# Performance work log

Hardware: AMD Instinct MI355X
Metric: run time of the kernel (lower is better)

Reference implementation:

```python
import jax, jax.numpy as jnp
import numpy as np

B, S, HID = 2, 2048, 2048
NH, NKV, HD = 16, 4, 128
MAXPOS = 2048


def _rope_tables(features, length, max_timescale=10000.0):
    fraction = jnp.arange(0, features, 2, dtype=jnp.float32) / features
    inv_freq = 1.0 / (max_timescale ** fraction)
    sinusoid = jnp.einsum('i,j->ij', jnp.arange(length, dtype=jnp.float32), inv_freq)
    sinusoid = jnp.concatenate([sinusoid, sinusoid], axis=-1)  # [length, features]
    return jnp.sin(sinusoid), jnp.cos(sinusoid)


def rotate_half(x):
    x1, x2 = jnp.split(x, 2, axis=-1)
    return jnp.concatenate([-x2, x1], axis=-1)


def setup_inputs() -> dict:
    key = jax.random.key(0)
    k1, k2, k3, k4, k5 = jax.random.split(key, 5)
    scale = 1.0 / np.sqrt(HID)
    hidden_states = jax.random.normal(k1, (B, S, HID), dtype=jnp.float32)
    Wq = jax.random.normal(k2, (NH * HD, HID), dtype=jnp.float32) * scale
    Wk = jax.random.normal(k3, (NKV * HD, HID), dtype=jnp.float32) * scale
    Wv = jax.random.normal(k4, (NKV * HD, HID), dtype=jnp.float32) * scale
    Wo = jax.random.normal(k5, (HID, NH * HD), dtype=jnp.float32) * scale
    # causal additive mask [B,1,S,S]
    neg = jnp.finfo(jnp.float32).min
    causal = jnp.where(jnp.tril(jnp.ones((S, S), dtype=bool)), 0.0, neg)
    attention_mask = jnp.broadcast_to(causal[None, None], (B, 1, S, S))
    sin, cos = _rope_tables(HD, MAXPOS)
    return {"hidden_states": hidden_states, "attention_mask": attention_mask,
            "Wq": Wq, "Wk": Wk, "Wv": Wv, "Wo": Wo, "sin": sin, "cos": cos}


def reference(hidden_states, attention_mask, Wq, Wk, Wv, Wo, sin, cos):
    bsz, qlen, _ = hidden_states.shape
    # projections (Linear, no bias): x @ W.T -> [B,S,heads,hd]
    q = (hidden_states @ Wq.T).reshape(bsz, qlen, NH, HD)
    k = (hidden_states @ Wk.T).reshape(bsz, qlen, NKV, HD)
    v = (hidden_states @ Wv.T).reshape(bsz, qlen, NKV, HD)
    # rotary embedding (applied in [B,S,H,D] layout)
    qcos = cos[:qlen][None, :, None, :]
    qsin = sin[:qlen][None, :, None, :]
    q = q * qcos + rotate_half(q) * qsin
    k = k * qcos + rotate_half(k) * qsin
    # GQA: repeat_kv equivalent via einsum grouping; expand kv heads to NH
    n_rep = NH // NKV
    q_g = q.reshape(bsz, qlen, NKV, n_rep, HD)  # group queries per kv head
    # scores: NOTE original applies no 1/sqrt(d) scaling
    scores = jnp.einsum('bqhrd,bkhd->bhrqk', q_g, k).reshape(bsz, NH, qlen, qlen)
    mask = attention_mask.at[:, :, :, 0].set(0.0)
    scores = scores + mask
    probs = jax.nn.softmax(scores.astype(jnp.float32), axis=-1).astype(q.dtype)
    probs_g = probs.reshape(bsz, NKV, n_rep, qlen, qlen)
    out = jnp.einsum('bhrqk,bkhd->bqhrd', probs_g, v).reshape(bsz, qlen, NH * HD)
    return out @ Wo.T
```

## Files before the change

kernel.cpp:

```cpp
#include <hip/hip_runtime.h>
#include <hip/hip_bf16.h>

typedef _Float16 f16x8 __attribute__((ext_vector_type(8)));
typedef __fp16 h16x2 __attribute__((ext_vector_type(2)));
typedef float f32x4 __attribute__((ext_vector_type(4)));
typedef float f32x16 __attribute__((ext_vector_type(16)));

#define B_    2
#define S_    2048
#define HID_  2048
#define NH_   16
#define NKV_  4
#define HD_   128
#define M_TOK 4096
#define NQKV  3072

#define MFMA16(a, b, c) __builtin_amdgcn_mfma_f32_16x16x32_f16(a, b, c, 0, 0, 0)
#define MFMA32(a, b, c) __builtin_amdgcn_mfma_f32_32x32x16_f16(a, b, c, 0, 0, 0)

union UW { unsigned u; h16x2 h; };

__device__ __forceinline__ unsigned short f2h(float f) {
  _Float16 h = (_Float16)f;
  return *(unsigned short*)&h;
}

__device__ __forceinline__ void gload_lds16(const unsigned short* g, unsigned short* l) {
  __builtin_amdgcn_global_load_lds((const __attribute__((address_space(1))) void*)g,
                                   (__attribute__((address_space(3))) void*)l,
                                   16, 0, 0);
}

__global__ void cast_f32_f16(const float* __restrict__ src, unsigned short* __restrict__ dst, int n4) {
  int i = blockIdx.x * blockDim.x + threadIdx.x;
  int stride = gridDim.x * blockDim.x;
  for (int idx = i; idx < n4; idx += stride) {
    float4 v = reinterpret_cast<const float4*>(src)[idx];
    ushort4 o;
    o.x = f2h(v.x); o.y = f2h(v.y); o.z = f2h(v.z); o.w = f2h(v.w);
    reinterpret_cast<ushort4*>(dst)[idx] = o;
  }
}

__global__ void cast_weights(const float* __restrict__ Wq, const float* __restrict__ Wk,
                             const float* __restrict__ Wv, const float* __restrict__ Wo,
                             unsigned short* __restrict__ dst) {
  const int n1 = 2048 * 2048 / 4, n2 = 512 * 2048 / 4;
  const int ntot = n1 * 2 + n2 * 2;
  int i = blockIdx.x * blockDim.x + threadIdx.x;
  int stride = gridDim.x * blockDim.x;
  for (int idx = i; idx < ntot; idx += stride) {
    const float* src; int off;
    if (idx < n1)                { src = Wq; off = idx; }
    else if (idx < n1 + n2)      { src = Wk; off = idx - n1; }
    else if (idx < n1 + 2 * n2)  { src = Wv; off = idx - n1 - n2; }
    else                         { src = Wo; off = idx - n1 - 2 * n2; }
    float4 v = reinterpret_cast<const float4*>(src)[off];
    ushort4 o;
    o.x = f2h(v.x); o.y = f2h(v.y); o.z = f2h(v.z); o.w = f2h(v.w);
    reinterpret_cast<ushort4*>(dst)[idx] = o;
  }
}

#define BM 128
#define BN 128
#define BK 32

template <bool OUT16>
__global__ __launch_bounds__(256) void gemm_bt_f16(
    const unsigned short* __restrict__ A, const unsigned short* __restrict__ Bm,
    void* __restrict__ Cv, int M, int N, int K) {
  __shared__ unsigned short As[BM * BK];
  __shared__ unsigned short Bs[BN * BK];
  const int tid  = threadIdx.x;
  const int lane = tid & 63;
  const int wave = tid >> 6;
  const int nbn  = N / BN;
  const int brow = (blockIdx.x / nbn) * BM;
  const int bcol = (blockIdx.x % nbn) * BN;
  const int wr = (wave >> 1) * 64;
  const int wc = (wave & 1) * 64;

  const int srow = wave * 16 + (lane >> 2);
  const int scol = (lane & 3) * 8;
  const unsigned short* ag = A + (size_t)(brow + srow) * K + scol;
  const unsigned short* bg = Bm + (size_t)(bcol + srow) * K + scol;
  unsigned short* aldsw = As + wave * 512;
  unsigned short* bldsw = Bs + wave * 512;

  f32x4 acc[4][4];
#pragma unroll
  for (int m = 0; m < 4; ++m)
#pragma unroll
    for (int n = 0; n < 4; ++n) acc[m][n] = (f32x4){0.f, 0.f, 0.f, 0.f};

  const int lr = lane & 15;
  const int lg = lane >> 4;

  for (int kt = 0; kt < K; kt += BK) {
    __syncthreads();
    gload_lds16(ag + kt, aldsw);
    gload_lds16(ag + (size_t)64 * K + kt, aldsw + 2048);
    gload_lds16(bg + kt, bldsw);
    gload_lds16(bg + (size_t)64 * K + kt, bldsw + 2048);
    __syncthreads();
    f16x8 af[4], bfr[4];
#pragma unroll
    for (int m = 0; m < 4; ++m)
      af[m] = *reinterpret_cast<const f16x8*>(&As[(wr + m * 16 + lr) * BK + lg * 8]);
#pragma unroll
    for (int n = 0; n < 4; ++n)
      bfr[n] = *reinterpret_cast<const f16x8*>(&Bs[(wc + n * 16 + lr) * BK + lg * 8]);
#pragma unroll
    for (int m = 0; m < 4; ++m)
#pragma unroll
      for (int n = 0; n < 4; ++n)
        acc[m][n] = MFMA16(af[m], bfr[n], acc[m][n]);
  }

#pragma unroll
  for (int m = 0; m < 4; ++m) {
#pragma unroll
    for (int r = 0; r < 4; ++r) {
      int row = brow + wr + m * 16 + lg * 4 + r;
      if (OUT16) {
        unsigned short* cp = (unsigned short*)Cv + (size_t)row * N + bcol + wc + lr;
#pragma unroll
        for (int n = 0; n < 4; ++n) cp[n * 16] = f2h(acc[m][n][r]);
      } else {
        float* cp = (float*)Cv + (size_t)row * N + bcol + wc + lr;
#pragma unroll
        for (int n = 0; n < 4; ++n) cp[n * 16] = acc[m][n][r];
      }
    }
  }
}

__global__ void rope_relayout(const unsigned short* __restrict__ QKV,
                              const float* __restrict__ sin_t, const float* __restrict__ cos_t,
                              unsigned short* __restrict__ Qo, unsigned short* __restrict__ Ko,
                              unsigned short* __restrict__ Vt) {
  int idx = blockIdx.x * blockDim.x + threadIdx.x;
  int d  = idx & 63;
  int t  = idx >> 6;
  int hh = t % 24;
  int bs = t / 24;
  int s  = bs & (S_ - 1);
  int b  = bs >> 11;
  const _Float16* xrow = (const _Float16*)QKV + (size_t)bs * NQKV;
  if (hh < 16) {
    float x0 = (float)xrow[hh * 128 + d], x1 = (float)xrow[hh * 128 + 64 + d];
    float c = cos_t[s * 128 + d], sn = sin_t[s * 128 + d];
    unsigned short* qp = Qo + (((size_t)(b * 16 + hh) * S_) + s) * 128 + d;
    qp[0]  = f2h(x0 * c - x1 * sn);
    qp[64] = f2h(x1 * c + x0 * sn);
  } else if (hh < 20) {
    int kvh = hh - 16;
    float x0 = (float)xrow[2048 + kvh * 128 + d], x1 = (float)xrow[2048 + kvh * 128 + 64 + d];
    float c = cos_t[s * 128 + d], sn = sin_t[s * 128 + d];
    unsigned short* kp = Ko + (((size_t)(b * 4 + kvh) * S_) + s) * 128 + d;
    kp[0]  = f2h(x0 * c - x1 * sn);
    kp[64] = f2h(x1 * c + x0 * sn);
  } else {
    int kvh = hh - 20;
    unsigned short x0 = QKV[(size_t)bs * NQKV + 2560 + kvh * 128 + d];
    unsigned short x1 = QKV[(size_t)bs * NQKV + 2560 + kvh * 128 + 64 + d];
    unsigned short* vp = Vt + ((size_t)(b * 4 + kvh) * 128 + d) * S_ + s;
    vp[0]        = x0;
    vp[64 * S_]  = x1;
  }
}

__global__ __launch_bounds__(256, 2) void flash_attn6(
    const unsigned short* __restrict__ Q, const unsigned short* __restrict__ Kk,
    const unsigned short* __restrict__ Vt, unsigned short* __restrict__ Ao) {
  __shared__ _Float16 Kl[2][64 * 128];
  __shared__ _Float16 Vl[2][128 * 64];
  const int lane = threadIdx.x & 63;
  const int w    = threadIdx.x >> 6;
  const int bh   = blockIdx.x & 31;
  const int bq   = 15 - (int)(blockIdx.x >> 5);
  const int b    = bh >> 4, h = bh & 15, kvh = h >> 2;
  const int q31  = lane & 31;
  const int hi   = lane >> 5;
  const int qb   = bq * 128;
  const int wqb  = qb + w * 32;
  const int qrow = wqb + q31;

  const _Float16* Qp = (const _Float16*)Q + (((size_t)(b * 16 + h) * S_) + qrow) * 128;
  const _Float16* Kp = (const _Float16*)Kk + ((size_t)(b * 4 + kvh) * S_) * 128;
  const _Float16* Vp = (const _Float16*)Vt + ((size_t)(b * 4 + kvh) * 128) * S_;

  f16x8 qf[8];
#pragma unroll
  for (int s = 0; s < 8; ++s) {
    f16x8 t = *reinterpret_cast<const f16x8*>(Qp + s * 16 + hi * 8);
#pragma unroll
    for (int j = 0; j < 8; ++j) t[j] = (_Float16)((float)t[j] * 1.44269504f);
    qf[s] = t;
  }

  f32x16 po0 = {}, po1 = {}, po2 = {}, po3 = {};
  float m = -1e30f, l = 0.f;

  const int krow = (lane >> 4);
  const int vrow = (lane >> 3);
  const int wklim = wqb + 32;
  const int nt = qb / 64 + 2;

#define STAGE(K0S, BUF)                                                               \
  {                                                                                   \
    unsigned short* kdst = (unsigned short*)Kl[BUF] + w * 2048;                       \
    unsigned short* vdst = (unsigned short*)Vl[BUF] + w * 2048;                       \
    _Pragma("unroll") for (int jj = 0; jj < 4; ++jj) {                                \
      const int j = w * 4 + jj;                                                       \
      const int kr = j * 4 + krow;                                                    \
      const int kc = (lane & 15) ^ (kr & 7);                                          \
      gload_lds16((const unsigned short*)(Kp + (size_t)((K0S) + kr) * 128 + kc * 8),  \
                  kdst + jj * 512);                                                   \
      const int vr = j * 8 + vrow;                                                    \
      const int vc = (lane & 7) ^ (vr & 7);                                           \
      gload_lds16((const unsigned short*)(Vp + (size_t)vr * S_ + (K0S) + vc * 8),     \
                  vdst + jj * 512);                                                   \
    }                                                                                 \
  }

  STAGE(0, 0)
  __syncthreads();

  int cur = 0;
  const int r7 = q31 & 7;
  for (int t = 0; t < nt; ++t) {
    const int k0 = t * 64;
    if (t + 1 < nt) STAGE((t + 1) * 64, cur ^ 1)

    if (k0 < wklim) {
      f32x16 s0 = {}, s1 = {};
      const _Float16* Kc = Kl[cur];
      __builtin_amdgcn_s_setprio(1);
#pragma unroll
      for (int s = 0; s < 8; ++s) {
        const int cc = (hi + 2 * s) ^ r7;
        f16x8 kf0 = *reinterpret_cast<const f16x8*>(Kc + q31 * 128 + cc * 8);
        f16x8 kf1 = *reinterpret_cast<const f16x8*>(Kc + (q31 + 32) * 128 + cc * 8);
        s0 = MFMA32(kf0, qf[s], s0);
        s1 = MFMA32(kf1, qf[s], s1);
      }
      __builtin_amdgcn_s_setprio(0);

      if (k0 + 63 > wqb) {
        int qrel = qrow - k0 - 4 * hi;
#pragma unroll
        for (int r = 0; r < 16; ++r) {
          int cr = (r & 3) + 8 * (r >> 2);
          if (cr > qrel)      s0[r] = -1e30f;
          if (cr + 32 > qrel) s1[r] = -1e30f;
        }
      }
      float tmx[8];
#pragma unroll
      for (int r = 0; r < 8; ++r)
        tmx[r] = fmaxf(fmaxf(s0[r], s0[r + 8]), fmaxf(s1[r], s1[r + 8]));
#pragma unroll
      for (int d = 4; d > 0; d >>= 1)
#pragma unroll
        for (int r = 0; r < d; ++r) tmx[r] = fmaxf(tmx[r], tmx[r + d]);
      float pmax = fmaxf(tmx[0], __shfl_xor(tmx[0], 32));
      if (__any(pmax > m + 8.0f)) {
        float mn = fmaxf(m, pmax);
        float sc = __builtin_amdgcn_exp2f(m - mn);
        l *= sc;
#pragma unroll
        for (int r = 0; r < 16; ++r) {
          po0[r] *= sc; po1[r] *= sc; po2[r] *= sc; po3[r] *= sc;
        }
        m = mn;
      }
#pragma unroll
      for (int r = 0; r < 16; ++r) s0[r] = __builtin_amdgcn_exp2f(s0[r] - m);
#pragma unroll
      for (int r = 0; r < 16; ++r) s1[r] = __builtin_amdgcn_exp2f(s1[r] - m);
      float u[8];
#pragma unroll
      for (int r = 0; r < 8; ++r)
        u[r] = (s0[r] + s0[r + 8]) + (s1[r] + s1[r + 8]);
#pragma unroll
      for (int d = 4; d > 0; d >>= 1)
#pragma unroll
        for (int r = 0; r < d; ++r) u[r] += u[r + d];
      l += u[0] + __shfl_xor(u[0], 32);

      f16x8 pa[4];
#pragma unroll
      for (int sl = 0; sl < 4; ++sl) {
        f32x16 sv = (sl < 2) ? s0 : s1;
        const int R = (sl & 1) * 8;
        UW w00, w01, w10, w11;
        w00.h = __builtin_amdgcn_cvt_pkrtz(sv[R + 0], sv[R + 1]);
        w01.h = __builtin_amdgcn_cvt_pkrtz(sv[R + 2], sv[R + 3]);
        w10.h = __builtin_amdgcn_cvt_pkrtz(sv[R + 4], sv[R + 5]);
        w11.h = __builtin_amdgcn_cvt_pkrtz(sv[R + 6], sv[R + 7]);
        unsigned x00 = __shfl_xor(w00.u, 32);
        unsigned x01 = __shfl_xor(w01.u, 32);
        unsigned x10 = __shfl_xor(w10.u, 32);
        unsigned x11 = __shfl_xor(w11.u, 32);
        UW W0, W1, W2, W3;
        W0.u = hi ? x10 : w00.u;
        W1.u = hi ? x11 : w01.u;
        W2.u = hi ? w10.u : x00;
        W3.u = hi ? w11.u : x01;
        union { unsigned uu[4]; f16x8 v; } pk;
        pk.uu[0] = W0.u; pk.uu[1] = W1.u; pk.uu[2] = W2.u; pk.uu[3] = W3.u;
        pa[sl] = pk.v;
      }

      const _Float16* Vc = Vl[cur];
      __builtin_amdgcn_s_setprio(1);
#pragma unroll
      for (int s = 0; s < 4; ++s) {
        const int cc = (hi + 2 * s) ^ r7;
        f16x8 vf0 = *reinterpret_cast<const f16x8*>(Vc + q31 * 64 + cc * 8);
        po0 = MFMA32(vf0, pa[s], po0);
        f16x8 vf1 = *reinterpret_cast<const f16x8*>(Vc + (q31 + 32) * 64 + cc * 8);
        po1 = MFMA32(vf1, pa[s], po1);
        f16x8 vf2 = *reinterpret_cast<const f16x8*>(Vc + (q31 + 64) * 64 + cc * 8);
        po2 = MFMA32(vf2, pa[s], po2);
        f16x8 vf3 = *reinterpret_cast<const f16x8*>(Vc + (q31 + 96) * 64 + cc * 8);
        po3 = MFMA32(vf3, pa[s], po3);
      }
      __builtin_amdgcn_s_setprio(0);
    }

    __syncthreads();
    cur ^= 1;
  }
#undef STAGE

  float inv = 1.0f / l;
  unsigned short* orow = Ao + ((size_t)(b * S_ + qrow)) * 2048 + h * 128;
#define STORE_DB(PO, DB)                                                          \
  {                                                                               \
    _Pragma("unroll") for (int a4 = 0; a4 < 4; ++a4) {                            \
      UW e0, e1;                                                                  \
      e0.h = __builtin_amdgcn_cvt_pkrtz(PO[4 * a4 + 0] * inv, PO[4 * a4 + 1] * inv); \
      e1.h = __builtin_amdgcn_cvt_pkrtz(PO[4 * a4 + 2] * inv, PO[4 * a4 + 3] * inv); \
      unsigned long long pv = ((unsigned long long)e1.u << 32) | e0.u;            \
      *reinterpret_cast<unsigned long long*>(orow + DB * 32 + a4 * 8 + hi * 4) = pv; \
    }                                                                             \
  }
  STORE_DB(po0, 0)
  STORE_DB(po1, 1)
  STORE_DB(po2, 2)
  STORE_DB(po3, 3)
#undef STORE_DB
}

extern "C" void kernel_launch(void* const* d_in, const int* in_sizes, int n_in,
                              void* d_out, int out_size, void* d_ws, size_t ws_size,
                              hipStream_t stream) {
  const float* hs    = (const float*)d_in[0];
  const float* Wq    = (const float*)d_in[2];
  const float* Wk    = (const float*)d_in[3];
  const float* Wv    = (const float*)d_in[4];
  const float* Wo    = (const float*)d_in[5];
  const float* sin_t = (const float*)d_in[6];
  const float* cos_t = (const float*)d_in[7];

  char* ws = (char*)d_ws;
  unsigned short* Xb    = (unsigned short*)ws; ws += (size_t)M_TOK * HID_ * 2;
  unsigned short* Wqkvb = (unsigned short*)ws; ws += (size_t)NQKV * HID_ * 2;
  unsigned short* Wob   = (unsigned short*)ws; ws += (size_t)HID_ * HID_ * 2;
  unsigned short* QKV   = (unsigned short*)ws; ws += (size_t)M_TOK * NQKV * 2;
  unsigned short* Qb    = (unsigned short*)ws; ws += (size_t)B_ * NH_ * S_ * HD_ * 2;
  unsigned short* Kb    = (unsigned short*)ws; ws += (size_t)B_ * NKV_ * S_ * HD_ * 2;
  unsigned short* Vtb   = (unsigned short*)ws; ws += (size_t)B_ * NKV_ * S_ * HD_ * 2;
  unsigned short* Aob   = (unsigned short*)ws; ws += (size_t)M_TOK * HID_ * 2;

  cast_f32_f16<<<2048, 256, 0, stream>>>(hs, Xb, M_TOK * HID_ / 4);
  cast_weights<<<2048, 256, 0, stream>>>(Wq, Wk, Wv, Wo, Wqkvb);

  gemm_bt_f16<true><<<(M_TOK / BM) * (NQKV / BN), 256, 0, stream>>>(Xb, Wqkvb, QKV, M_TOK, NQKV, HID_);

  rope_relayout<<<(B_ * S_ * 24 * 64) / 256, 256, 0, stream>>>(QKV, sin_t, cos_t, Qb, Kb, Vtb);

  flash_attn6<<<512, 256, 0, stream>>>(Qb, Kb, Vtb, Aob);

  gemm_bt_f16<false><<<(M_TOK / BM) * (HID_ / BN), 256, 0, stream>>>(Aob, Wob, d_out, M_TOK, HID_, HID_);
}
```

Measured before the change: 248.9 us.

## Double GEMM K-tile to 64 and interleave flash-attention query block order

```diff
diff --git a/kernel.cpp b/kernel.cpp
--- a/kernel.cpp
+++ b/kernel.cpp
@@ -64,7 +64,7 @@
 
 #define BM 128
 #define BN 128
-#define BK 32
+#define BK 64
 
 template <bool OUT16>
 __global__ __launch_bounds__(256) void gemm_bt_f16(
@@ -80,42 +80,47 @@
   const int bcol = (blockIdx.x % nbn) * BN;
   const int wr = (wave >> 1) * 64;
   const int wc = (wave & 1) * 64;
-
-  const int srow = wave * 16 + (lane >> 2);
-  const int scol = (lane & 3) * 8;
-  const unsigned short* ag = A + (size_t)(brow + srow) * K + scol;
-  const unsigned short* bg = Bm + (size_t)(bcol + srow) * K + scol;
-  unsigned short* aldsw = As + wave * 512;
-  unsigned short* bldsw = Bs + wave * 512;
-
-  f32x4 acc[4][4];
-#pragma unroll
-  for (int m = 0; m < 4; ++m)
-#pragma unroll
-    for (int n = 0; n < 4; ++n) acc[m][n] = (f32x4){0.f, 0.f, 0.f, 0.f};
-
   const int lr = lane & 15;
   const int lg = lane >> 4;
 
+  f32x4 acc[4][4];
+#pragma unroll
+  for (int m = 0; m < 4; ++m)
+#pragma unroll
+    for (int n = 0; n < 4; ++n) acc[m][n] = (f32x4){0.f, 0.f, 0.f, 0.f};
+
   for (int kt = 0; kt < K; kt += BK) {
     __syncthreads();
-    gload_lds16(ag + kt, aldsw);
-    gload_lds16(ag + (size_t)64 * K + kt, aldsw + 2048);
-    gload_lds16(bg + kt, bldsw);
-    gload_lds16(bg + (size_t)64 * K + kt, bldsw + 2048);
+#pragma unroll
+    for (int ch = 0; ch < 4; ++ch) {
+      const int G = ch * 256 + tid;
+      const int r = G >> 3, g = G & 7;
+      gload_lds16(A + (size_t)(brow + r) * K + kt + g * 8, As + (ch * 256 + wave * 64) * 8);
+      gload_lds16(Bm + (size_t)(bcol + r) * K + kt + g * 8, Bs + (ch * 256 + wave * 64) * 8);
+    }
     __syncthreads();
-    f16x8 af[4], bfr[4];
-#pragma unroll
-    for (int m = 0; m < 4; ++m)
-      af[m] = *reinterpret_cast<const f16x8*>(&As[(wr + m * 16 + lr) * BK + lg * 8]);
-#pragma unroll
-    for (int n = 0; n < 4; ++n)
-      bfr[n] = *reinterpret_cast<const f16x8*>(&Bs[(wc + n * 16 + lr) * BK + lg * 8]);
-#pragma unroll
-    for (int m = 0; m < 4; ++m)
-#pragma unroll
-      for (int n = 0; n < 4; ++n)
-        acc[m][n] = MFMA16(af[m], bfr[n], acc[m][n]);
+    f16x8 af[4][2], bfr[4][2];
+#pragma unroll
+    for (int m = 0; m < 4; ++m) {
+      const int row = wr + m * 16 + lr;
+#pragma unroll
+      for (int ks = 0; ks < 2; ++ks)
+        af[m][ks] = *reinterpret_cast<const f16x8*>(&As[row * BK + ks * 32 + lg * 8]);
+    }
+#pragma unroll
+    for (int n = 0; n < 4; ++n) {
+      const int row = wc + n * 16 + lr;
+#pragma unroll
+      for (int ks = 0; ks < 2; ++ks)
+        bfr[n][ks] = *reinterpret_cast<const f16x8*>(&Bs[row * BK + ks * 32 + lg * 8]);
+    }
+#pragma unroll
+    for (int ks = 0; ks < 2; ++ks)
+#pragma unroll
+      for (int m = 0; m < 4; ++m)
+#pragma unroll
+        for (int n = 0; n < 4; ++n)
+          acc[m][n] = MFMA16(af[m][ks], bfr[n][ks], acc[m][n]);
   }
 
 #pragma unroll
@@ -179,7 +184,8 @@
   const int lane = threadIdx.x & 63;
   const int w    = threadIdx.x >> 6;
   const int bh   = blockIdx.x & 31;
-  const int bq   = 15 - (int)(blockIdx.x >> 5);
+  const int j    = (int)(blockIdx.x >> 5);
+  const int bq   = (j < 8) ? (15 - j) : (j - 8);
   const int b    = bh >> 4, h = bh & 15, kvh = h >> 2;
   const int q31  = lane & 31;
   const int hi   = lane >> 5;
@@ -196,7 +202,7 @@
   for (int s = 0; s < 8; ++s) {
     f16x8 t = *reinterpret_cast<const f16x8*>(Qp + s * 16 + hi * 8);
 #pragma unroll
-    for (int j = 0; j < 8; ++j) t[j] = (_Float16)((float)t[j] * 1.44269504f);
+    for (int jj = 0; jj < 8; ++jj) t[jj] = (_Float16)((float)t[jj] * 1.44269504f);
     qf[s] = t;
   }
 
@@ -213,12 +219,12 @@
     unsigned short* kdst = (unsigned short*)Kl[BUF] + w * 2048;                       \
     unsigned short* vdst = (unsigned short*)Vl[BUF] + w * 2048;                       \
     _Pragma("unroll") for (int jj = 0; jj < 4; ++jj) {                                \
-      const int j = w * 4 + jj;                                                       \
-      const int kr = j * 4 + krow;                                                    \
+      const int jx = w * 4 + jj;                                                      \
+      const int kr = jx * 4 + krow;                                                   \
       const int kc = (lane & 15) ^ (kr & 7);                                          \
       gload_lds16((const unsigned short*)(Kp + (size_t)((K0S) + kr) * 128 + kc * 8),  \
                   kdst + jj * 512);                                                   \
-      const int vr = j * 8 + vrow;                                                    \
+      const int vr = jx * 8 + vrow;                                                   \
       const int vc = (lane & 7) ^ (vr & 7);                                           \
       gload_lds16((const unsigned short*)(Vp + (size_t)vr * S_ + (K0S) + vc * 8),     \
                   vdst + jj * 512);                                                   \
```

After: 258.2 us. +3.7%, slower.
